# Kernel optimization log

Hardware: AMD Instinct MI355X
Metric: run time of the kernel (lower is better)

Reference implementation:

```python
import jax, jax.numpy as jnp
import numpy as np

N = 8
PI = 3.1415  # module uses this approximation, not math.pi
Q = 50

T_LUMA = np.array([[16,11,10,16,24,40,51,61],[12,12,14,19,26,58,60,55],[14,13,16,24,40,57,69,56],[14,17,22,29,51,87,80,62],[18,22,37,56,68,109,103,77],[24,35,55,64,81,104,113,92],[49,64,78,87,103,121,120,101],[72,92,95,98,112,100,103,99]], dtype=np.float32)
Q_CHROMA = np.array([[17,18,24,47,99,99,99,99],[18,21,26,66,99,99,99,99],[24,26,56,99,99,99,99,99],[47,66,99,99,99,99,99,99],[99,99,99,99,99,99,99,99],[99,99,99,99,99,99,99,99],[99,99,99,99,99,99,99,99],[99,99,99,99,99,99,99,99]], dtype=np.float32)


def _zigzag(n):
    # faithful port of the module's zigzag(); returns pattern.T (row-major)
    p = np.zeros((n, n), dtype=np.int64)
    tri = lambda v: v * (v + 1) // 2
    for y in range(n):
        for x in range(y % 2, n - y, 2):
            p[y, x] = tri(x + y + 1) - x - 1
    for y in range(n):
        for x in range((y + 1) % 2, n - y, 2):
            p[y, x] = tri(x + y + 1) - y - 1
    for y in range(n - 1, -1, -1):
        for x in range(n - 1, -1 + (n - y), -1):
            p[y, x] = n * n - 1 - p[n - y - 1, n - x - 1]
    return p.T.copy()


def _constants():
    t = np.arange(N, dtype=np.float32)
    # C8[u, y] = cos((y/N) * (u + 0.5) * PI)  -- same basis as the conv weight
    C8 = np.cos(np.outer((t + 0.5) * PI, t / N)).astype(np.float32)
    norm = np.ones((N, N), dtype=np.float32)
    norm[:, 0] = np.sqrt(2.0) / 2
    norm[0, :] = np.sqrt(2.0) / 2
    norm /= 4.0
    s = 5000.0 / Q if Q < 50 else 200 - 2 * Q
    Q_luma = np.floor((s * T_LUMA + 50) / 100)
    qvec = 1.0 / np.concatenate([Q_luma.ravel(), Q_CHROMA.ravel(), Q_CHROMA.ravel()]).astype(np.float32)
    z = _zigzag(N).ravel()
    inv_perm = np.argsort(z)  # zigzag conv scatters: out[z[i]] = in[i]
    return jnp.asarray(C8), jnp.asarray(norm), jnp.asarray(qvec, jnp.float32), jnp.asarray(inv_perm)

_C8, _NORM, _QVEC, _INVP = _constants()


def setup_inputs() -> dict:
    key = jax.random.key(0)
    x = jax.random.normal(key, (32, 3, 512, 512), dtype=jnp.float32)
    return {"x": x}


def reference(x):
    B, C, H, W = x.shape
    # split into N x N blocks: (B, C, Hb, N, Wb, N)
    blocks = x.reshape(B, C, H // N, N, W // N, N)
    # 2D block DCT: coef[a,u] = sum_{y,x} block[y,x] * C8[a,y] * C8[u,x]
    coef = jnp.einsum('bchywx,ay,ux->bcauhw', blocks, _C8, _C8)
    # diagonal normalization (norm conv == per-frequency scale)
    coef = coef * _NORM[None, None, :, :, None, None]
    coef = coef.reshape(B, C, N * N, H // N, W // N)
    # zigzag permutation conv == channel gather
    coef = jnp.take(coef, _INVP, axis=2)
    # quantization conv == diagonal per-channel scale over C*N*N channels
    out = coef.reshape(B, C * N * N, H // N, W // N) * _QVEC[None, :, None, None]
    return out
```

## Files before the change

### kernel.cpp

```cpp
#include <hip/hip_runtime.h>


#define PI_F 3.1415f

__device__ __constant__ int QTAB[2][64] = {
    {16,11,10,16,24,40,51,61,
     12,12,14,19,26,58,60,55,
     14,13,16,24,40,57,69,56,
     14,17,22,29,51,87,80,62,
     18,22,37,56,68,109,103,77,
     24,35,55,64,81,104,113,92,
     49,64,78,87,103,121,120,101,
     72,92,95,98,112,100,103,99},
    {17,18,24,47,99,99,99,99,
     18,21,26,66,99,99,99,99,
     24,26,56,99,99,99,99,99,
     47,66,99,99,99,99,99,99,
     99,99,99,99,99,99,99,99,
     99,99,99,99,99,99,99,99,
     99,99,99,99,99,99,99,99,
     99,99,99,99,99,99,99,99}
};

__global__ __launch_bounds__(256)
void DCTCompression_25786983645730_kernel(const float* __restrict__ x,
                                          float* __restrict__ out) {
    __shared__ float sC8[64];
    __shared__ float sScale[64];
    __shared__ int   sZoff[64];

    const int tid = threadIdx.x;
    const int idx = blockIdx.x;
    const int hbg = idx & 15;
    const int bc  = idx >> 4;
    const int c   = bc % 3;

    if (tid == 0) {
        int p[64];
        for (int y = 0; y < 8; ++y)
            for (int xx = (y & 1); xx < 8 - y; xx += 2) {
                int v = xx + y + 1;
                p[y * 8 + xx] = v * (v + 1) / 2 - xx - 1;
            }
        for (int y = 0; y < 8; ++y)
            for (int xx = ((y + 1) & 1); xx < 8 - y; xx += 2) {
                int v = xx + y + 1;
                p[y * 8 + xx] = v * (v + 1) / 2 - y - 1;
            }
        for (int y = 7; y >= 0; --y)
            for (int xx = 7; xx >= 8 - y; --xx)
                p[y * 8 + xx] = 63 - p[(7 - y) * 8 + (7 - xx)];
        const int* qt = QTAB[(c == 0) ? 0 : 1];
        for (int i = 0; i < 64; ++i) {
            int a = i >> 3, u = i & 7;
            int zi = p[u * 8 + a];
            sZoff[i] = zi << 12;
            float nrm = (a == 0 || u == 0) ? 0.17677669529663687f : 0.25f;
            sScale[i] = nrm / (float)qt[zi];
        }
    }
    if (tid < 64) {
        int u = tid >> 3, y = tid & 7;
        sC8[tid] = cosf(((float)u + 0.5f) * PI_F * ((float)y * 0.125f));
    }
    __syncthreads();

    const int wave = tid >> 6;
    const int wb   = tid & 63;
    const int hb   = hbg * 4 + wave;

    const float* xb = x + ((size_t)bc * 512 + (size_t)hb * 8) * 512 + wb * 8;
    float* ob = out + (size_t)bc * 64 * 4096 + hb * 64 + wb;

    float4 r[8][2];
#pragma unroll
    for (int y = 0; y < 8; ++y) {
        r[y][0] = *reinterpret_cast<const float4*>(xb + y * 512);
        r[y][1] = *reinterpret_cast<const float4*>(xb + y * 512 + 4);
    }

    float tmp[8][8];
#pragma unroll
    for (int a = 0; a < 8; ++a)
#pragma unroll
        for (int xx = 0; xx < 8; ++xx) tmp[a][xx] = 0.0f;

#pragma unroll
    for (int y = 0; y < 8; ++y) {
        float row[8] = {r[y][0].x, r[y][0].y, r[y][0].z, r[y][0].w,
                        r[y][1].x, r[y][1].y, r[y][1].z, r[y][1].w};
#pragma unroll
        for (int a = 0; a < 8; ++a) {
            float cv = sC8[a * 8 + y];
#pragma unroll
            for (int xx = 0; xx < 8; ++xx)
                tmp[a][xx] = fmaf(cv, row[xx], tmp[a][xx]);
        }
    }

#pragma unroll
    for (int a = 0; a < 8; ++a) {
#pragma unroll
        for (int u = 0; u < 8; ++u) {
            float acc = 0.0f;
#pragma unroll
            for (int xx = 0; xx < 8; ++xx)
                acc = fmaf(tmp[a][xx], sC8[u * 8 + xx], acc);
            int j = a * 8 + u;
            ob[sZoff[j]] = acc * sScale[j];
        }
    }
}

extern "C" void kernel_launch(void* const* d_in, const int* in_sizes, int n_in,
                              void* d_out, int out_size, void* d_ws, size_t ws_size,
                              hipStream_t stream) {
    const float* x = (const float*)d_in[0];
    float* out = (float*)d_out;
    DCTCompression_25786983645730_kernel<<<dim3(1536), dim3(256), 0, stream>>>(x, out);
}
```

Before: 184.2 us.

## Precompute DCT tables in init kernel, stream row-pass, use nontemporal stores

Moves the per-block serial table setup (zigzag, scales, cosine basis) into a tiny init kernel that writes the tables to workspace, so the main kernel no longer has a single-thread prologue or a __syncthreads. The main kernel reads the tables through uniform global loads, computes the row pass one output row at a time to cut live registers, sets an occupancy hint of 6 blocks per CU, and writes outputs with nontemporal stores. The trade-offs are an extra kernel launch and table reads from global/scalar cache instead of LDS.

```diff
diff --git a/kernel.cpp b/kernel.cpp
--- a/kernel.cpp
+++ b/kernel.cpp
@@ -22,55 +22,57 @@
      99,99,99,99,99,99,99,99}
 };
 
-__global__ __launch_bounds__(256)
+__global__ void dct_init_kernel(float* __restrict__ ws) {
+    const int tid = threadIdx.x;
+    const int u = tid >> 3, y = tid & 7;
+    ws[tid] = cosf(((float)u + 0.5f) * PI_F * ((float)y * 0.125f));
+    if (tid == 0) {
+        int p[64];
+        for (int yy = 0; yy < 8; ++yy)
+            for (int xx = (yy & 1); xx < 8 - yy; xx += 2) {
+                int v = xx + yy + 1;
+                p[yy * 8 + xx] = v * (v + 1) / 2 - xx - 1;
+            }
+        for (int yy = 0; yy < 8; ++yy)
+            for (int xx = ((yy + 1) & 1); xx < 8 - yy; xx += 2) {
+                int v = xx + yy + 1;
+                p[yy * 8 + xx] = v * (v + 1) / 2 - yy - 1;
+            }
+        for (int yy = 7; yy >= 0; --yy)
+            for (int xx = 7; xx >= 8 - yy; --xx)
+                p[yy * 8 + xx] = 63 - p[(7 - yy) * 8 + (7 - xx)];
+        int* zoff = (int*)(ws + 192);
+        for (int i = 0; i < 64; ++i) {
+            int a = i >> 3, uu = i & 7;
+            int zi = p[uu * 8 + a];
+            zoff[i] = zi << 12;
+            float nrm = (a == 0 || uu == 0) ? 0.17677669529663687f : 0.25f;
+            ws[64 + i]  = nrm / (float)QTAB[0][zi];
+            ws[128 + i] = nrm / (float)QTAB[1][zi];
+        }
+    }
+}
+
+__global__ __launch_bounds__(256, 6)
 void DCTCompression_25786983645730_kernel(const float* __restrict__ x,
-                                          float* __restrict__ out) {
-    __shared__ float sC8[64];
-    __shared__ float sScale[64];
-    __shared__ int   sZoff[64];
-
+                                          float* __restrict__ out,
+                                          const float* __restrict__ ws) {
     const int tid = threadIdx.x;
     const int idx = blockIdx.x;
     const int hbg = idx & 15;
     const int bc  = idx >> 4;
     const int c   = bc % 3;
 
-    if (tid == 0) {
-        int p[64];
-        for (int y = 0; y < 8; ++y)
-            for (int xx = (y & 1); xx < 8 - y; xx += 2) {
-                int v = xx + y + 1;
-                p[y * 8 + xx] = v * (v + 1) / 2 - xx - 1;
-            }
-        for (int y = 0; y < 8; ++y)
-            for (int xx = ((y + 1) & 1); xx < 8 - y; xx += 2) {
-                int v = xx + y + 1;
-                p[y * 8 + xx] = v * (v + 1) / 2 - y - 1;
-            }
-        for (int y = 7; y >= 0; --y)
-            for (int xx = 7; xx >= 8 - y; --xx)
-                p[y * 8 + xx] = 63 - p[(7 - y) * 8 + (7 - xx)];
-        const int* qt = QTAB[(c == 0) ? 0 : 1];
-        for (int i = 0; i < 64; ++i) {
-            int a = i >> 3, u = i & 7;
-            int zi = p[u * 8 + a];
-            sZoff[i] = zi << 12;
-            float nrm = (a == 0 || u == 0) ? 0.17677669529663687f : 0.25f;
-            sScale[i] = nrm / (float)qt[zi];
-        }
-    }
-    if (tid < 64) {
-        int u = tid >> 3, y = tid & 7;
-        sC8[tid] = cosf(((float)u + 0.5f) * PI_F * ((float)y * 0.125f));
-    }
-    __syncthreads();
+    const float* __restrict__ cb   = ws;
+    const float* __restrict__ sc   = (c == 0) ? ws + 64 : ws + 128;
+    const int*   __restrict__ zoff = (const int*)(ws + 192);
 
     const int wave = tid >> 6;
     const int wb   = tid & 63;
     const int hb   = hbg * 4 + wave;
 
     const float* xb = x + ((size_t)bc * 512 + (size_t)hb * 8) * 512 + wb * 8;
-    float* ob = out + (size_t)bc * 64 * 4096 + hb * 64 + wb;
+    float* ob = out + (size_t)bc * 262144 + hb * 64 + wb;
 
     float4 r[8][2];
 #pragma unroll
@@ -79,35 +81,29 @@
         r[y][1] = *reinterpret_cast<const float4*>(xb + y * 512 + 4);
     }
 
-    float tmp[8][8];
-#pragma unroll
-    for (int a = 0; a < 8; ++a)
-#pragma unroll
-        for (int xx = 0; xx < 8; ++xx) tmp[a][xx] = 0.0f;
-
-#pragma unroll
-    for (int y = 0; y < 8; ++y) {
-        float row[8] = {r[y][0].x, r[y][0].y, r[y][0].z, r[y][0].w,
-                        r[y][1].x, r[y][1].y, r[y][1].z, r[y][1].w};
-#pragma unroll
-        for (int a = 0; a < 8; ++a) {
-            float cv = sC8[a * 8 + y];
-#pragma unroll
-            for (int xx = 0; xx < 8; ++xx)
-                tmp[a][xx] = fmaf(cv, row[xx], tmp[a][xx]);
-        }
-    }
-
 #pragma unroll
     for (int a = 0; a < 8; ++a) {
+        float tmp[8] = {0, 0, 0, 0, 0, 0, 0, 0};
+#pragma unroll
+        for (int y = 0; y < 8; ++y) {
+            float cv = cb[a * 8 + y];
+            tmp[0] = fmaf(cv, r[y][0].x, tmp[0]);
+            tmp[1] = fmaf(cv, r[y][0].y, tmp[1]);
+            tmp[2] = fmaf(cv, r[y][0].z, tmp[2]);
+            tmp[3] = fmaf(cv, r[y][0].w, tmp[3]);
+            tmp[4] = fmaf(cv, r[y][1].x, tmp[4]);
+            tmp[5] = fmaf(cv, r[y][1].y, tmp[5]);
+            tmp[6] = fmaf(cv, r[y][1].z, tmp[6]);
+            tmp[7] = fmaf(cv, r[y][1].w, tmp[7]);
+        }
 #pragma unroll
         for (int u = 0; u < 8; ++u) {
-            float acc = 0.0f;
+            float acc = tmp[0] * cb[u * 8 + 0];
 #pragma unroll
-            for (int xx = 0; xx < 8; ++xx)
-                acc = fmaf(tmp[a][xx], sC8[u * 8 + xx], acc);
-            int j = a * 8 + u;
-            ob[sZoff[j]] = acc * sScale[j];
+            for (int xx = 1; xx < 8; ++xx)
+                acc = fmaf(tmp[xx], cb[u * 8 + xx], acc);
+            const int j = a * 8 + u;
+            __builtin_nontemporal_store(acc * sc[j], ob + zoff[j]);
         }
     }
 }
@@ -117,5 +113,7 @@
                               hipStream_t stream) {
     const float* x = (const float*)d_in[0];
     float* out = (float*)d_out;
-    DCTCompression_25786983645730_kernel<<<dim3(1536), dim3(256), 0, stream>>>(x, out);
+    float* ws = (float*)d_ws;
+    dct_init_kernel<<<dim3(1), dim3(64), 0, stream>>>(ws);
+    DCTCompression_25786983645730_kernel<<<dim3(1536), dim3(256), 0, stream>>>(x, out, ws);
 }
```

New measurement: 202.7 us. 10.0% more time.

## Precompute tables at compile time and stage outputs through LDS for vector stores

Applied to the files above, without the earlier changes.

Moves the zigzag permutation and quantization scale tables into constexpr tables, which removes the serial single-thread setup and its barrier stall from each block. Output coefficients are staged in shared memory in two passes so each wave writes contiguous float4 rows per zigzag channel, replacing scattered scalar stores. The block index is also remapped across batch-channel planes, and launch bounds request higher occupancy. The cost is extra shared memory, two more barriers per pass, and register pressure from holding 64 coefficients per thread.

```diff
diff --git a/kernel.cpp b/kernel.cpp
--- a/kernel.cpp
+++ b/kernel.cpp
@@ -3,62 +3,61 @@
 
 #define PI_F 3.1415f
 
-__device__ __constant__ int QTAB[2][64] = {
-    {16,11,10,16,24,40,51,61,
-     12,12,14,19,26,58,60,55,
-     14,13,16,24,40,57,69,56,
-     14,17,22,29,51,87,80,62,
-     18,22,37,56,68,109,103,77,
-     24,35,55,64,81,104,113,92,
-     49,64,78,87,103,121,120,101,
-     72,92,95,98,112,100,103,99},
-    {17,18,24,47,99,99,99,99,
-     18,21,26,66,99,99,99,99,
-     24,26,56,99,99,99,99,99,
-     47,66,99,99,99,99,99,99,
-     99,99,99,99,99,99,99,99,
-     99,99,99,99,99,99,99,99,
-     99,99,99,99,99,99,99,99,
-     99,99,99,99,99,99,99,99}
+struct Tables {
+    int   z[64];
+    float scl[2][64];
 };
 
-__global__ __launch_bounds__(256)
+constexpr Tables make_tables() {
+    Tables t{};
+    int p[64] = {};
+    for (int y = 0; y < 8; ++y)
+        for (int x = (y & 1); x < 8 - y; x += 2) {
+            int v = x + y + 1;
+            p[y * 8 + x] = v * (v + 1) / 2 - x - 1;
+        }
+    for (int y = 0; y < 8; ++y)
+        for (int x = ((y + 1) & 1); x < 8 - y; x += 2) {
+            int v = x + y + 1;
+            p[y * 8 + x] = v * (v + 1) / 2 - y - 1;
+        }
+    for (int y = 7; y >= 0; --y)
+        for (int x = 7; x >= 8 - y; --x)
+            p[y * 8 + x] = 63 - p[(7 - y) * 8 + (7 - x)];
+    const int QT[2][64] = {
+        {16,11,10,16,24,40,51,61, 12,12,14,19,26,58,60,55,
+         14,13,16,24,40,57,69,56, 14,17,22,29,51,87,80,62,
+         18,22,37,56,68,109,103,77, 24,35,55,64,81,104,113,92,
+         49,64,78,87,103,121,120,101, 72,92,95,98,112,100,103,99},
+        {17,18,24,47,99,99,99,99, 18,21,26,66,99,99,99,99,
+         24,26,56,99,99,99,99,99, 47,66,99,99,99,99,99,99,
+         99,99,99,99,99,99,99,99, 99,99,99,99,99,99,99,99,
+         99,99,99,99,99,99,99,99, 99,99,99,99,99,99,99,99}
+    };
+    for (int i = 0; i < 64; ++i) {
+        int a = i >> 3, u = i & 7;
+        int zi = p[u * 8 + a];
+        t.z[i] = zi;
+        float nrm = (a == 0 || u == 0) ? 0.17677669529663687f : 0.25f;
+        t.scl[0][i] = nrm / (float)QT[0][zi];
+        t.scl[1][i] = nrm / (float)QT[1][zi];
+    }
+    return t;
+}
+constexpr Tables TBL = make_tables();
+
+__global__ __launch_bounds__(256, 4)
 void DCTCompression_25786983645730_kernel(const float* __restrict__ x,
                                           float* __restrict__ out) {
     __shared__ float sC8[64];
-    __shared__ float sScale[64];
-    __shared__ int   sZoff[64];
+    __shared__ float st[32][256];
 
     const int tid = threadIdx.x;
-    const int idx = blockIdx.x;
-    const int hbg = idx & 15;
-    const int bc  = idx >> 4;
-    const int c   = bc % 3;
+    const int k   = blockIdx.x >> 3;
+    const int bc  = (blockIdx.x & 7) * 12 + (k >> 4);
+    const int hbg = k & 15;
+    const int lc  = ((bc % 3) != 0);
 
-    if (tid == 0) {
-        int p[64];
-        for (int y = 0; y < 8; ++y)
-            for (int xx = (y & 1); xx < 8 - y; xx += 2) {
-                int v = xx + y + 1;
-                p[y * 8 + xx] = v * (v + 1) / 2 - xx - 1;
-            }
-        for (int y = 0; y < 8; ++y)
-            for (int xx = ((y + 1) & 1); xx < 8 - y; xx += 2) {
-                int v = xx + y + 1;
-                p[y * 8 + xx] = v * (v + 1) / 2 - y - 1;
-            }
-        for (int y = 7; y >= 0; --y)
-            for (int xx = 7; xx >= 8 - y; --xx)
-                p[y * 8 + xx] = 63 - p[(7 - y) * 8 + (7 - xx)];
-        const int* qt = QTAB[(c == 0) ? 0 : 1];
-        for (int i = 0; i < 64; ++i) {
-            int a = i >> 3, u = i & 7;
-            int zi = p[u * 8 + a];
-            sZoff[i] = zi << 12;
-            float nrm = (a == 0 || u == 0) ? 0.17677669529663687f : 0.25f;
-            sScale[i] = nrm / (float)qt[zi];
-        }
-    }
     if (tid < 64) {
         int u = tid >> 3, y = tid & 7;
         sC8[tid] = cosf(((float)u + 0.5f) * PI_F * ((float)y * 0.125f));
@@ -66,12 +65,10 @@
     __syncthreads();
 
     const int wave = tid >> 6;
-    const int wb   = tid & 63;
+    const int lane = tid & 63;
     const int hb   = hbg * 4 + wave;
 
-    const float* xb = x + ((size_t)bc * 512 + (size_t)hb * 8) * 512 + wb * 8;
-    float* ob = out + (size_t)bc * 64 * 4096 + hb * 64 + wb;
-
+    const float* xb = x + ((size_t)bc * 512 + (size_t)hb * 8) * 512 + lane * 8;
     float4 r[8][2];
 #pragma unroll
     for (int y = 0; y < 8; ++y) {
@@ -79,36 +76,52 @@
         r[y][1] = *reinterpret_cast<const float4*>(xb + y * 512 + 4);
     }
 
-    float tmp[8][8];
+    float c64[64];
 #pragma unroll
-    for (int a = 0; a < 8; ++a)
+    for (int a = 0; a < 8; ++a) {
+        float tmp[8] = {0, 0, 0, 0, 0, 0, 0, 0};
 #pragma unroll
-        for (int xx = 0; xx < 8; ++xx) tmp[a][xx] = 0.0f;
-
+        for (int y = 0; y < 8; ++y) {
+            float cv = sC8[a * 8 + y];
+            tmp[0] = fmaf(cv, r[y][0].x, tmp[0]);
+            tmp[1] = fmaf(cv, r[y][0].y, tmp[1]);
+            tmp[2] = fmaf(cv, r[y][0].z, tmp[2]);
+            tmp[3] = fmaf(cv, r[y][0].w, tmp[3]);
+            tmp[4] = fmaf(cv, r[y][1].x, tmp[4]);
+            tmp[5] = fmaf(cv, r[y][1].y, tmp[5]);
+            tmp[6] = fmaf(cv, r[y][1].z, tmp[6]);
+            tmp[7] = fmaf(cv, r[y][1].w, tmp[7]);
+        }
 #pragma unroll
-    for (int y = 0; y < 8; ++y) {
-        float row[8] = {r[y][0].x, r[y][0].y, r[y][0].z, r[y][0].w,
-                        r[y][1].x, r[y][1].y, r[y][1].z, r[y][1].w};
+        for (int u = 0; u < 8; ++u) {
+            float acc = tmp[0] * sC8[u * 8 + 0];
 #pragma unroll
-        for (int a = 0; a < 8; ++a) {
-            float cv = sC8[a * 8 + y];
-#pragma unroll
-            for (int xx = 0; xx < 8; ++xx)
-                tmp[a][xx] = fmaf(cv, row[xx], tmp[a][xx]);
+            for (int xx = 1; xx < 8; ++xx)
+                acc = fmaf(tmp[xx], sC8[u * 8 + xx], acc);
+            const int j = a * 8 + u;
+            const float s0 = TBL.scl[0][j], s1 = TBL.scl[1][j];
+            c64[j] = acc * (lc ? s1 : s0);
         }
     }
 
+    float* ob = out + (size_t)bc * 262144 + (size_t)hbg * 256 + lane * 4;
+
 #pragma unroll
-    for (int a = 0; a < 8; ++a) {
+    for (int pass = 0; pass < 2; ++pass) {
 #pragma unroll
-        for (int u = 0; u < 8; ++u) {
-            float acc = 0.0f;
+        for (int j = 0; j < 64; ++j) {
+            const int zi = TBL.z[j];
+            if ((zi >> 5) == pass)
+                st[zi & 31][(wave << 6) | lane] = c64[j];
+        }
+        __syncthreads();
 #pragma unroll
-            for (int xx = 0; xx < 8; ++xx)
-                acc = fmaf(tmp[a][xx], sC8[u * 8 + xx], acc);
-            int j = a * 8 + u;
-            ob[sZoff[j]] = acc * sScale[j];
+        for (int i = 0; i < 8; ++i) {
+            const int zl = i * 4 + wave;
+            float4 v = *reinterpret_cast<const float4*>(&st[zl][lane * 4]);
+            *reinterpret_cast<float4*>(ob + (size_t)(pass * 32 + zl) * 4096) = v;
         }
+        __syncthreads();
     }
 }
 
```

After: 215.6 us. 17.0% more time.
